# Kernel tuning notes

Hardware: AMD Instinct MI355X
Metric: run time of the kernel (lower is better)

The kernel has to match this reference:

```python
import jax, jax.numpy as jnp
import numpy as np

BETA = 0.25
K = 1024   # num_codebook_vectors
D = 256    # latent_dim


def setup_inputs() -> dict:
    key = jax.random.key(0)
    k1, k2 = jax.random.split(key)
    z = jax.random.normal(k1, (32, D, 32, 32), dtype=jnp.float32)
    # original init: uniform(-1/K, 1/K)
    codebook = jax.random.uniform(k2, (K, D), dtype=jnp.float32, minval=-1.0 / K, maxval=1.0 / K)
    return {"z": z, "codebook": codebook}


def reference(z, codebook):
    B, C, H, W = z.shape
    sg = jax.lax.stop_gradient
    # NCHW -> NHWC, flatten to [N, D]
    z_nhwc = jnp.transpose(z, (0, 2, 3, 1))
    zf = z_nhwc.reshape(-1, C)
    # squared distances via sum-of-squares + matmul: [N, K]
    d = (jnp.sum(zf * zf, axis=1, keepdims=True)
         + jnp.sum(codebook * codebook, axis=1)
         - 2.0 * jnp.matmul(zf, codebook.T))
    idx = jnp.argmin(d, axis=1)                      # [N]
    z_q = codebook[idx].reshape(B, H, W, C)          # gather + reshape
    # commitment + codebook loss
    loss = (jnp.mean((sg(z_q) - z_nhwc) ** 2)
            + BETA * jnp.mean((z_q - sg(z_nhwc)) ** 2))
    # straight-through estimator
    z_q = z_nhwc + sg(z_q - z_nhwc)
    z_q = jnp.transpose(z_q, (0, 3, 1, 2))           # back to NCHW
    return z_q, idx, loss
```

## Files before the change

kernel.cpp:

```cpp
#include <hip/hip_runtime.h>

constexpr int D_ = 256;
constexpr int K_ = 1024;
constexpr int P_ = 1024;
constexpr int N_ = 32768;

constexpr int IDX_OFF  = 8388608;
constexpr int LOSS_OFF = 8421376;

constexpr int CB16_OFF = 0;
constexpr int CN_OFF   = 262400;
constexpr int ZN_OFF   = 263424;
constexpr int CNT_OFF  = 296448;
constexpr int WL_OFF   = 296449;
constexpr size_t SCRATCH_BYTES = (size_t)(WL_OFF + N_) * 4;

constexpr float RESCUE_MARGIN = 1e-4f;

typedef _Float16 half8 __attribute__((ext_vector_type(8)));
typedef float f32x4 __attribute__((ext_vector_type(4)));

__device__ __forceinline__ void stage16(const float* g, float* l) {
  __builtin_amdgcn_global_load_lds(
      (const __attribute__((address_space(1))) unsigned int*)g,
      (__attribute__((address_space(3))) unsigned int*)l, 16, 0, 0);
}

__global__ __launch_bounds__(64) void vq_prep(const float* __restrict__ z,
                                              const float* __restrict__ cb,
                                              float* __restrict__ scratch,
                                              float* __restrict__ loss) {
  const int blk = blockIdx.x;
  const int lane = threadIdx.x;
  if (blk < 512) {
    const int n0 = blk * 64;
    const int b = n0 >> 10, p0 = n0 & (P_ - 1);
    const float* zp = z + (size_t)b * (D_ * P_) + p0 + lane;
    float a8[8];
    #pragma unroll
    for (int i = 0; i < 8; ++i) a8[i] = 0.0f;
    for (int oct = 0; oct < 32; ++oct) {
      #pragma unroll
      for (int i = 0; i < 8; ++i) {
        float v = zp[(size_t)(oct * 8 + i) * P_];
        a8[i] = fmaf(v, v, a8[i]);
      }
    }
    scratch[ZN_OFF + n0 + lane] = ((a8[0] + a8[1]) + (a8[2] + a8[3])) +
                                  ((a8[4] + a8[5]) + (a8[6] + a8[7]));
    if (blk == 0 && lane == 0) {
      *loss = 0.0f;
      ((int*)(scratch + CNT_OFF))[0] = 0;
    }
  } else if (blk < 1536) {
    const int k = blk - 512;
    const float* row = cb + (size_t)k * D_;
    double s = 0.0;
    #pragma unroll
    for (int i = 0; i < 4; ++i) {
      double v = (double)row[lane + i * 64];
      s = fma(v, v, s);
    }
    #pragma unroll
    for (int off = 32; off; off >>= 1) s += __shfl_down(s, off, 64);
    if (lane == 0) scratch[CN_OFF + k] = (float)s;
  } else {
    const int kt = blk - 1536;
    const int k = kt * 16 + (lane & 15);
    const int quad = lane >> 4;
    _Float16* cw = (_Float16*)(scratch + CB16_OFF);
    for (int ds = 0; ds < 8; ++ds) {
      const float* src = cb + (size_t)k * D_ + ds * 32 + quad * 8;
      half8 h, lo;
      #pragma unroll
      for (int j = 0; j < 8; ++j) {
        const float v = src[j] * 1024.0f;
        const _Float16 hh = (_Float16)v;
        h[j] = hh;
        lo[j] = (_Float16)(v - (float)hh);
      }
      const int s = kt * 8 + ds;
      *(half8*)(cw + ((size_t)(s * 2 + 0) * 64 + lane) * 8) = h;
      *(half8*)(cw + ((size_t)(s * 2 + 1) * 64 + lane) * 8) = lo;
    }
  }
}

__global__ __launch_bounds__(256, 2) void vq_mfma(const float* __restrict__ z,
                                                  const float* __restrict__ scratch_c,
                                                  float* __restrict__ scratch,
                                                  float* __restrict__ idxf) {
  const int t = threadIdx.x;
  const int w = t >> 6;
  const int l = t & 63;
  const int quad = l >> 4;
  const int col = l & 15;
  const int rh = w & 1;
  const int cs = w >> 1;
  const int n0 = blockIdx.x * 64;
  const int b = n0 >> 10;
  const int p0 = n0 & (P_ - 1);

  const float* __restrict__ cbsw_f = scratch_c + CB16_OFF;
  const float* __restrict__ cnorm = scratch_c + CN_OFF;
  const float* __restrict__ zn = scratch_c + ZN_OFF;

  __shared__ alignas(16) float Bbuf[2][2][4096];
  __shared__ alignas(16) float cnLds[1024];
  __shared__ float sM1[4][32];
  __shared__ float sM2[4][32];
  __shared__ int   sI1[4][32];
  float* Azs = &Bbuf[0][1][0];

  *(float4*)(cnLds + t * 4) = *(const float4*)(cnorm + t * 4);

  float znr[2][4];
  #pragma unroll
  for (int rt = 0; rt < 2; ++rt) {
    const float4 znv = *(const float4*)(zn + n0 + rh * 32 + rt * 16 + quad * 4);
    znr[rt][0] = znv.x; znr[rt][1] = znv.y;
    znr[rt][2] = znv.z; znr[rt][3] = znv.w;
  }

  half8 Ah[2][8], Al[2][8];
  const int dl0 = w * 8;
  for (int ds = 0; ds < 8; ++ds) {
    __syncthreads();
    #pragma unroll
    for (int i = 0; i < 8; ++i) {
      const int dloc = dl0 + i;
      Azs[l * 33 + dloc] =
          z[(size_t)b * (D_ * P_) + (size_t)(ds * 32 + dloc) * P_ + p0 + l];
    }
    __syncthreads();
    #pragma unroll
    for (int rt = 0; rt < 2; ++rt) {
      const float* src = &Azs[(rh * 32 + rt * 16 + col) * 33 + quad * 8];
      half8 h, lo;
      #pragma unroll
      for (int j = 0; j < 8; ++j) {
        const float v = src[j];
        const _Float16 hh = (_Float16)v;
        h[j] = hh;
        lo[j] = (_Float16)(v - (float)hh);
      }
      Ah[rt][ds] = h;
      Al[rt][ds] = lo;
    }
  }

  asm volatile("s_waitcnt vmcnt(0)" ::: "memory");

  const int ch0 = rh * 8;
  const float* gsbase = cbsw_f + (size_t)cs * 32 * 4096 + l * 4;
  #pragma unroll
  for (int j = 0; j < 8; ++j) {
    const int chunk = ch0 + j;
    stage16(gsbase + chunk * 256, &Bbuf[cs][0][chunk * 256]);
  }

  float m1[2][4], m2v[2][4];
  int i1[2][4];
  #pragma unroll
  for (int rt = 0; rt < 2; ++rt)
    #pragma unroll
    for (int r = 0; r < 4; ++r) { m1[rt][r] = 1e30f; m2v[rt][r] = 1e30f; i1[rt][r] = 0; }

  float* bcur = &Bbuf[cs][0][0];
  float* bnxt = &Bbuf[cs][1][0];
  const float* cnp = cnLds + cs * 512 + col;
  int kg = cs * 512 + col;

  f32x4 AH0, AM0, AL0, AH1, AM1, AL1;
  f32x4 BH0, BM0, BL0, BH1, BM1, BL1;
  float cnfA = 0.f, cnfB = 0.f;
  int kgA = 0, kgB = 0;

  auto do_phase = [&](f32x4& H0, f32x4& M0, f32x4& L0,
                      f32x4& H1, f32x4& M1, f32x4& L1,
                      int p, float& cnf_sav, int& kg_sav) {
    asm volatile("s_waitcnt vmcnt(0)" ::: "memory");
    __builtin_amdgcn_s_barrier();
    __builtin_amdgcn_sched_barrier(0);

    if (p < 31) {
      const float* gsp = gsbase + (size_t)(p + 1) * 4096;
      #pragma unroll
      for (int j = 0; j < 8; ++j) {
        const int chunk = ch0 + j;
        stage16(gsp + chunk * 256, bnxt + chunk * 256);
      }
    }

    cnf_sav = *cnp;
    kg_sav = kg;

    H0 = {0.f,0.f,0.f,0.f}; M0 = {0.f,0.f,0.f,0.f}; L0 = {0.f,0.f,0.f,0.f};
    H1 = {0.f,0.f,0.f,0.f}; M1 = {0.f,0.f,0.f,0.f}; L1 = {0.f,0.f,0.f,0.f};

    __builtin_amdgcn_s_setprio(1);
    #pragma unroll
    for (int ds = 0; ds < 8; ++ds) {
      const half8 bh = *(const half8*)(bcur + (ds * 2 + 0) * 256 + l * 4);
      const half8 bl = *(const half8*)(bcur + (ds * 2 + 1) * 256 + l * 4);
      H0 = __builtin_amdgcn_mfma_f32_16x16x32_f16(Ah[0][ds], bh, H0, 0, 0, 0);
      H1 = __builtin_amdgcn_mfma_f32_16x16x32_f16(Ah[1][ds], bh, H1, 0, 0, 0);
      M0 = __builtin_amdgcn_mfma_f32_16x16x32_f16(Ah[0][ds], bl, M0, 0, 0, 0);
      M1 = __builtin_amdgcn_mfma_f32_16x16x32_f16(Ah[1][ds], bl, M1, 0, 0, 0);
      L0 = __builtin_amdgcn_mfma_f32_16x16x32_f16(Al[0][ds], bh, L0, 0, 0, 0);
      L1 = __builtin_amdgcn_mfma_f32_16x16x32_f16(Al[1][ds], bh, L1, 0, 0, 0);
    }
    __builtin_amdgcn_s_setprio(0);

    cnp += 16;
    kg += 16;
    float* tmp = bcur; bcur = bnxt; bnxt = tmp;
  };

  auto do_argmin = [&](const f32x4& H0, const f32x4& M0, const f32x4& L0,
                       const f32x4& H1, const f32x4& M1, const f32x4& L1,
                       float cnf, int kgp) {
    #pragma unroll
    for (int r = 0; r < 4; ++r) {
      const float s0 = fmaf((H0[r] + M0[r]) + L0[r], -0x1p-9f, znr[0][r] + cnf);
      if (s0 < m1[0][r]) { m2v[0][r] = m1[0][r]; m1[0][r] = s0; i1[0][r] = kgp; }
      else if (s0 < m2v[0][r]) m2v[0][r] = s0;
      const float s1 = fmaf((H1[r] + M1[r]) + L1[r], -0x1p-9f, znr[1][r] + cnf);
      if (s1 < m1[1][r]) { m2v[1][r] = m1[1][r]; m1[1][r] = s1; i1[1][r] = kgp; }
      else if (s1 < m2v[1][r]) m2v[1][r] = s1;
    }
  };

  do_phase(AH0, AM0, AL0, AH1, AM1, AL1, 0, cnfA, kgA);
  for (int i = 0; i < 15; ++i) {
    do_phase(BH0, BM0, BL0, BH1, BM1, BL1, 2 * i + 1, cnfB, kgB);
    do_argmin(AH0, AM0, AL0, AH1, AM1, AL1, cnfA, kgA);
    do_phase(AH0, AM0, AL0, AH1, AM1, AL1, 2 * i + 2, cnfA, kgA);
    do_argmin(BH0, BM0, BL0, BH1, BM1, BL1, cnfB, kgB);
  }
  do_phase(BH0, BM0, BL0, BH1, BM1, BL1, 31, cnfB, kgB);
  do_argmin(AH0, AM0, AL0, AH1, AM1, AL1, cnfA, kgA);
  do_argmin(BH0, BM0, BL0, BH1, BM1, BL1, cnfB, kgB);

  #pragma unroll
  for (int off = 1; off <= 8; off <<= 1) {
    #pragma unroll
    for (int rt = 0; rt < 2; ++rt)
      #pragma unroll
      for (int r = 0; r < 4; ++r) {
        const float o1 = __shfl_xor(m1[rt][r], off, 64);
        const float o2 = __shfl_xor(m2v[rt][r], off, 64);
        const int oi = __shfl_xor(i1[rt][r], off, 64);
        if (o1 < m1[rt][r]) { m2v[rt][r] = fminf(m1[rt][r], o2); m1[rt][r] = o1; i1[rt][r] = oi; }
        else if (o1 == m1[rt][r]) { i1[rt][r] = min(i1[rt][r], oi); m2v[rt][r] = m1[rt][r]; }
        else { m2v[rt][r] = fminf(m2v[rt][r], o1); }
      }
  }

  if (col == 0) {
    #pragma unroll
    for (int rt = 0; rt < 2; ++rt)
      #pragma unroll
      for (int r = 0; r < 4; ++r) {
        const int rl = rt * 16 + quad * 4 + r;
        sM1[w][rl] = m1[rt][r];
        sM2[w][rl] = m2v[rt][r];
        sI1[w][rl] = i1[rt][r];
      }
  }
  __syncthreads();
  if (w < 2 && col == 0) {
    int* cnt = (int*)(scratch + CNT_OFF);
    int* wl = (int*)(scratch + WL_OFF);
    #pragma unroll
    for (int rt = 0; rt < 2; ++rt)
      #pragma unroll
      for (int r = 0; r < 4; ++r) {
        const int rl = rt * 16 + quad * 4 + r;
        float a1 = sM1[w][rl], a2 = sM2[w][rl];
        int ai = sI1[w][rl];
        const float o1 = sM1[w + 2][rl], o2 = sM2[w + 2][rl];
        const int oi = sI1[w + 2][rl];
        if (o1 < a1) { a2 = fminf(a1, o2); a1 = o1; ai = oi; }
        else if (o1 == a1) { ai = min(ai, oi); a2 = a1; }
        else { a2 = fminf(a2, o1); }
        const int n = n0 + w * 32 + rl;
        idxf[n] = (float)ai;
        if (a2 - a1 < RESCUE_MARGIN) {
          const int pos = atomicAdd(cnt, 1);
          wl[pos] = n;
        }
      }
  }
}

__global__ __launch_bounds__(256, 4) void vq_rescue(const float* __restrict__ z,
                                                    const float* __restrict__ cb,
                                                    const float* __restrict__ scratch,
                                                    float* __restrict__ idxf) {
  const int tid = threadIdx.x;
  const float* cnorm = scratch + CN_OFF;
  const float* zn = scratch + ZN_OFF;
  const int count = ((const int*)(scratch + CNT_OFF))[0];
  const int* wl = (const int*)(scratch + WL_OFF);

  __shared__ alignas(16) float zb[8][D_];
  __shared__ int nrow[8];
  __shared__ float rv[256];
  __shared__ int ri[256];

  for (int base = blockIdx.x * 8; base < count; base += gridDim.x * 8) {
    const int take = min(8, count - base);
    if (tid < 8) nrow[tid] = wl[base + (tid < take ? tid : 0)];
    __syncthreads();
    #pragma unroll
    for (int r = 0; r < 8; ++r) {
      const int n = nrow[r];
      const int b = n >> 10, p = n & (P_ - 1);
      zb[r][tid] = z[(size_t)b * (D_ * P_) + (size_t)tid * P_ + p];
    }
    __syncthreads();

    const int k0 = tid * 4;
    const float4* __restrict__ cr0 = (const float4*)(cb + (size_t)(k0 + 0) * D_);
    const float4* __restrict__ cr1 = (const float4*)(cb + (size_t)(k0 + 1) * D_);
    const float4* __restrict__ cr2 = (const float4*)(cb + (size_t)(k0 + 2) * D_);
    const float4* __restrict__ cr3 = (const float4*)(cb + (size_t)(k0 + 3) * D_);

    float acc[8][4];
    #pragma unroll
    for (int r = 0; r < 8; ++r)
      #pragma unroll
      for (int j = 0; j < 4; ++j) acc[r][j] = 0.0f;

    for (int d4 = 0; d4 < 64; ++d4) {
      const float4 v0 = cr0[d4], v1 = cr1[d4], v2 = cr2[d4], v3 = cr3[d4];
      #pragma unroll
      for (int r = 0; r < 8; ++r) {
        const float4 zv = ((const float4*)zb[r])[d4];
        acc[r][0] = fmaf(zv.x, v0.x, acc[r][0]);
        acc[r][0] = fmaf(zv.y, v0.y, acc[r][0]);
        acc[r][0] = fmaf(zv.z, v0.z, acc[r][0]);
        acc[r][0] = fmaf(zv.w, v0.w, acc[r][0]);
        acc[r][1] = fmaf(zv.x, v1.x, acc[r][1]);
        acc[r][1] = fmaf(zv.y, v1.y, acc[r][1]);
        acc[r][1] = fmaf(zv.z, v1.z, acc[r][1]);
        acc[r][1] = fmaf(zv.w, v1.w, acc[r][1]);
        acc[r][2] = fmaf(zv.x, v2.x, acc[r][2]);
        acc[r][2] = fmaf(zv.y, v2.y, acc[r][2]);
        acc[r][2] = fmaf(zv.z, v2.z, acc[r][2]);
        acc[r][2] = fmaf(zv.w, v2.w, acc[r][2]);
        acc[r][3] = fmaf(zv.x, v3.x, acc[r][3]);
        acc[r][3] = fmaf(zv.y, v3.y, acc[r][3]);
        acc[r][3] = fmaf(zv.z, v3.z, acc[r][3]);
        acc[r][3] = fmaf(zv.w, v3.w, acc[r][3]);
      }
    }

    for (int r = 0; r < 8; ++r) {
      const int n = nrow[r];
      const float zA = zn[n];
      float bv = 1e30f;
      int bi = 0x7fffffff;
      #pragma unroll
      for (int j = 0; j < 4; ++j) {
        const float A = zA + cnorm[k0 + j];
        const float s = A - 2.0f * acc[r][j];
        if (s < bv) { bv = s; bi = k0 + j; }
      }
      rv[tid] = bv; ri[tid] = bi;
      __syncthreads();
      for (int off = 128; off >= 1; off >>= 1) {
        if (tid < off) {
          const float ov = rv[tid + off];
          const int oi = ri[tid + off];
          if (ov < rv[tid] || (ov == rv[tid] && oi < ri[tid])) { rv[tid] = ov; ri[tid] = oi; }
        }
        __syncthreads();
      }
      if (tid == 0 && r < take) idxf[n] = (float)ri[0];
      __syncthreads();
    }
  }
}

__global__ __launch_bounds__(256) void vq_gather(const float* __restrict__ z,
                                                 const float* __restrict__ cb,
                                                 const float* __restrict__ idxf,
                                                 float* __restrict__ out,
                                                 float* __restrict__ loss) {
  const int tid = threadIdx.x;
  const int lane = tid & 63;
  const int w = tid >> 6;
  const int n0 = blockIdx.x * 64;
  const int b = n0 >> 10;
  const int p0 = n0 & (P_ - 1);
  const int p = p0 + lane;

  const int idx = (int)(idxf[n0 + lane] + 0.5f);
  const float4* crow4 = (const float4*)(cb + (size_t)idx * D_);
  const size_t base = (size_t)b * (D_ * P_) + p;

  float acc = 0.0f;
  #pragma unroll 4
  for (int ci = 0; ci < 16; ++ci) {
    const float4 v = crow4[w * 16 + ci];
    const int c = w * 64 + ci * 4;
    const float vv[4] = {v.x, v.y, v.z, v.w};
    #pragma unroll
    for (int u = 0; u < 4; ++u) {
      const size_t a = base + (size_t)(c + u) * P_;
      const float zv = z[a];
      const float d = vv[u] - zv;
      out[a] = zv + d;
      acc = fmaf(d, d, acc);
    }
  }
  #pragma unroll
  for (int off = 32; off; off >>= 1) acc += __shfl_down(acc, off, 64);
  __shared__ float wsum[4];
  if (lane == 0) wsum[w] = acc;
  __syncthreads();
  if (tid == 0) {
    float s = wsum[0] + wsum[1] + wsum[2] + wsum[3];
    atomicAdd(loss, s * (1.25f / 8388608.0f));
  }
}

extern "C" void kernel_launch(void* const* d_in, const int* in_sizes, int n_in,
                              void* d_out, int out_size, void* d_ws, size_t ws_size,
                              hipStream_t stream) {
  const float* z = (const float*)d_in[0];
  const float* cb = (const float*)d_in[1];
  float* out = (float*)d_out;

  float* scratch = (d_ws != nullptr && ws_size >= SCRATCH_BYTES)
                       ? (float*)d_ws : out;

  vq_prep<<<1600, 64, 0, stream>>>(z, cb, scratch, out + LOSS_OFF);
  vq_mfma<<<N_ / 64, 256, 0, stream>>>(z, scratch, scratch, out + IDX_OFF);
  vq_rescue<<<128, 256, 0, stream>>>(z, cb, scratch, out + IDX_OFF);
  vq_gather<<<N_ / 64, 256, 0, stream>>>(z, cb, out + IDX_OFF, out, out + LOSS_OFF);
}
```

Baseline: 227.5 us.

## Give each wave private double-buffered codebook staging and drop block barriers

Each wave gets its own LDS ping-pong buffer pair and stages its codebook slice itself, in half-tiles, synchronising with a per-wave vmcnt wait instead of a workgroup-wide s_barrier every phase. The two-accumulator-set software pipeline that overlapped the argmin of one tile with the MFMAs of the next is replaced by a simple loop that computes a tile and then immediately does its argmin. The intent is to remove inter-wave barrier stalls. In exchange, the waves that used to share a buffer now each load their own copy, doubling global/L2 codebook traffic, and the argmin is no longer overlapped with the MFMAs.

```diff
diff --git a/kernel.cpp b/kernel.cpp
--- a/kernel.cpp
+++ b/kernel.cpp
@@ -105,12 +105,12 @@
   const float* __restrict__ cnorm = scratch_c + CN_OFF;
   const float* __restrict__ zn = scratch_c + ZN_OFF;
 
-  __shared__ alignas(16) float Bbuf[2][2][4096];
+  __shared__ alignas(16) float Bw[4][2][2048];
   __shared__ alignas(16) float cnLds[1024];
   __shared__ float sM1[4][32];
   __shared__ float sM2[4][32];
   __shared__ int   sI1[4][32];
-  float* Azs = &Bbuf[0][1][0];
+  float* Azs = &Bw[0][0][0];
 
   *(float4*)(cnLds + t * 4) = *(const float4*)(cnorm + t * 4);
 
@@ -148,16 +148,15 @@
       Al[rt][ds] = lo;
     }
   }
-
+  __syncthreads();
   asm volatile("s_waitcnt vmcnt(0)" ::: "memory");
 
-  const int ch0 = rh * 8;
-  const float* gsbase = cbsw_f + (size_t)cs * 32 * 4096 + l * 4;
+  float* myb0 = &Bw[w][0][0];
+  float* myb1 = &Bw[w][1][0];
+  const float* gs = cbsw_f + (size_t)cs * 32 * 4096 + l * 4;
+
   #pragma unroll
-  for (int j = 0; j < 8; ++j) {
-    const int chunk = ch0 + j;
-    stage16(gsbase + chunk * 256, &Bbuf[cs][0][chunk * 256]);
-  }
+  for (int j = 0; j < 8; ++j) stage16(gs + j * 256, myb0 + j * 256);
 
   float m1[2][4], m2v[2][4];
   int i1[2][4];
@@ -166,81 +165,74 @@
     #pragma unroll
     for (int r = 0; r < 4; ++r) { m1[rt][r] = 1e30f; m2v[rt][r] = 1e30f; i1[rt][r] = 0; }
 
-  float* bcur = &Bbuf[cs][0][0];
-  float* bnxt = &Bbuf[cs][1][0];
   const float* cnp = cnLds + cs * 512 + col;
   int kg = cs * 512 + col;
 
-  f32x4 AH0, AM0, AL0, AH1, AM1, AL1;
-  f32x4 BH0, BM0, BL0, BH1, BM1, BL1;
-  float cnfA = 0.f, cnfB = 0.f;
-  int kgA = 0, kgB = 0;
-
-  auto do_phase = [&](f32x4& H0, f32x4& M0, f32x4& L0,
-                      f32x4& H1, f32x4& M1, f32x4& L1,
-                      int p, float& cnf_sav, int& kg_sav) {
-    asm volatile("s_waitcnt vmcnt(0)" ::: "memory");
-    __builtin_amdgcn_s_barrier();
-    __builtin_amdgcn_sched_barrier(0);
-
-    if (p < 31) {
-      const float* gsp = gsbase + (size_t)(p + 1) * 4096;
-      #pragma unroll
-      for (int j = 0; j < 8; ++j) {
-        const int chunk = ch0 + j;
-        stage16(gsp + chunk * 256, bnxt + chunk * 256);
-      }
-    }
-
-    cnf_sav = *cnp;
-    kg_sav = kg;
-
-    H0 = {0.f,0.f,0.f,0.f}; M0 = {0.f,0.f,0.f,0.f}; L0 = {0.f,0.f,0.f,0.f};
-    H1 = {0.f,0.f,0.f,0.f}; M1 = {0.f,0.f,0.f,0.f}; L1 = {0.f,0.f,0.f,0.f};
-
-    __builtin_amdgcn_s_setprio(1);
-    #pragma unroll
-    for (int ds = 0; ds < 8; ++ds) {
-      const half8 bh = *(const half8*)(bcur + (ds * 2 + 0) * 256 + l * 4);
-      const half8 bl = *(const half8*)(bcur + (ds * 2 + 1) * 256 + l * 4);
-      H0 = __builtin_amdgcn_mfma_f32_16x16x32_f16(Ah[0][ds], bh, H0, 0, 0, 0);
-      H1 = __builtin_amdgcn_mfma_f32_16x16x32_f16(Ah[1][ds], bh, H1, 0, 0, 0);
-      M0 = __builtin_amdgcn_mfma_f32_16x16x32_f16(Ah[0][ds], bl, M0, 0, 0, 0);
-      M1 = __builtin_amdgcn_mfma_f32_16x16x32_f16(Ah[1][ds], bl, M1, 0, 0, 0);
-      L0 = __builtin_amdgcn_mfma_f32_16x16x32_f16(Al[0][ds], bh, L0, 0, 0, 0);
-      L1 = __builtin_amdgcn_mfma_f32_16x16x32_f16(Al[1][ds], bh, L1, 0, 0, 0);
-    }
-    __builtin_amdgcn_s_setprio(0);
-
-    cnp += 16;
-    kg += 16;
-    float* tmp = bcur; bcur = bnxt; bnxt = tmp;
-  };
-
-  auto do_argmin = [&](const f32x4& H0, const f32x4& M0, const f32x4& L0,
-                       const f32x4& H1, const f32x4& M1, const f32x4& L1,
-                       float cnf, int kgp) {
-    #pragma unroll
-    for (int r = 0; r < 4; ++r) {
-      const float s0 = fmaf((H0[r] + M0[r]) + L0[r], -0x1p-9f, znr[0][r] + cnf);
-      if (s0 < m1[0][r]) { m2v[0][r] = m1[0][r]; m1[0][r] = s0; i1[0][r] = kgp; }
-      else if (s0 < m2v[0][r]) m2v[0][r] = s0;
-      const float s1 = fmaf((H1[r] + M1[r]) + L1[r], -0x1p-9f, znr[1][r] + cnf);
-      if (s1 < m1[1][r]) { m2v[1][r] = m1[1][r]; m1[1][r] = s1; i1[1][r] = kgp; }
-      else if (s1 < m2v[1][r]) m2v[1][r] = s1;
-    }
-  };
-
-  do_phase(AH0, AM0, AL0, AH1, AM1, AL1, 0, cnfA, kgA);
-  for (int i = 0; i < 15; ++i) {
-    do_phase(BH0, BM0, BL0, BH1, BM1, BL1, 2 * i + 1, cnfB, kgB);
-    do_argmin(AH0, AM0, AL0, AH1, AM1, AL1, cnfA, kgA);
-    do_phase(AH0, AM0, AL0, AH1, AM1, AL1, 2 * i + 2, cnfA, kgA);
-    do_argmin(BH0, BM0, BL0, BH1, BM1, BL1, cnfB, kgB);
-  }
-  do_phase(BH0, BM0, BL0, BH1, BM1, BL1, 31, cnfB, kgB);
-  do_argmin(AH0, AM0, AL0, AH1, AM1, AL1, cnfA, kgA);
-  do_argmin(BH0, BM0, BL0, BH1, BM1, BL1, cnfB, kgB);
+  for (int kt = 0; kt < 32; ++kt) {
+    f32x4 H0 = {0.f,0.f,0.f,0.f}, M0 = {0.f,0.f,0.f,0.f}, L0 = {0.f,0.f,0.f,0.f};
+    f32x4 H1 = {0.f,0.f,0.f,0.f}, M1 = {0.f,0.f,0.f,0.f}, L1 = {0.f,0.f,0.f,0.f};
+
+    {
+      const float* gsp = gs + (size_t)(kt * 2 + 1) * 2048;
+      #pragma unroll
+      for (int j = 0; j < 8; ++j) stage16(gsp + j * 256, myb1 + j * 256);
+      asm volatile("s_waitcnt vmcnt(8)" ::: "memory");
+      __builtin_amdgcn_sched_barrier(0);
+
+      __builtin_amdgcn_s_setprio(1);
+      #pragma unroll
+      for (int ds = 0; ds < 4; ++ds) {
+        const half8 bh = *(const half8*)(myb0 + (ds * 2 + 0) * 256 + l * 4);
+        const half8 bl = *(const half8*)(myb0 + (ds * 2 + 1) * 256 + l * 4);
+        H0 = __builtin_amdgcn_mfma_f32_16x16x32_f16(Ah[0][ds], bh, H0, 0, 0, 0);
+        H1 = __builtin_amdgcn_mfma_f32_16x16x32_f16(Ah[1][ds], bh, H1, 0, 0, 0);
+        M0 = __builtin_amdgcn_mfma_f32_16x16x32_f16(Ah[0][ds], bl, M0, 0, 0, 0);
+        M1 = __builtin_amdgcn_mfma_f32_16x16x32_f16(Ah[1][ds], bl, M1, 0, 0, 0);
+        L0 = __builtin_amdgcn_mfma_f32_16x16x32_f16(Al[0][ds], bh, L0, 0, 0, 0);
+        L1 = __builtin_amdgcn_mfma_f32_16x16x32_f16(Al[1][ds], bh, L1, 0, 0, 0);
+      }
+      __builtin_amdgcn_s_setprio(0);
+    }
+
+    {
+      if (kt < 31) {
+        const float* gsp = gs + (size_t)(kt * 2 + 2) * 2048;
+        #pragma unroll
+        for (int j = 0; j < 8; ++j) stage16(gsp + j * 256, myb0 + j * 256);
+        asm volatile("s_waitcnt vmcnt(8)" ::: "memory");
+      } else {
+        asm volatile("s_waitcnt vmcnt(0)" ::: "memory");
+      }
+      __builtin_amdgcn_sched_barrier(0);
+
+      __builtin_amdgcn_s_setprio(1);
+      #pragma unroll
+      for (int ds = 4; ds < 8; ++ds) {
+        const half8 bh = *(const half8*)(myb1 + ((ds - 4) * 2 + 0) * 256 + l * 4);
+        const half8 bl = *(const half8*)(myb1 + ((ds - 4) * 2 + 1) * 256 + l * 4);
+        H0 = __builtin_amdgcn_mfma_f32_16x16x32_f16(Ah[0][ds], bh, H0, 0, 0, 0);
+        H1 = __builtin_amdgcn_mfma_f32_16x16x32_f16(Ah[1][ds], bh, H1, 0, 0, 0);
+        M0 = __builtin_amdgcn_mfma_f32_16x16x32_f16(Ah[0][ds], bl, M0, 0, 0, 0);
+        M1 = __builtin_amdgcn_mfma_f32_16x16x32_f16(Ah[1][ds], bl, M1, 0, 0, 0);
+        L0 = __builtin_amdgcn_mfma_f32_16x16x32_f16(Al[0][ds], bh, L0, 0, 0, 0);
+        L1 = __builtin_amdgcn_mfma_f32_16x16x32_f16(Al[1][ds], bh, L1, 0, 0, 0);
+      }
+      __builtin_amdgcn_s_setprio(0);
+
+      const float cnf = *cnp;
+      #pragma unroll
+      for (int r = 0; r < 4; ++r) {
+        const float s0 = fmaf((H0[r] + M0[r]) + L0[r], -0x1p-9f, znr[0][r] + cnf);
+        if (s0 < m1[0][r]) { m2v[0][r] = m1[0][r]; m1[0][r] = s0; i1[0][r] = kg; }
+        else if (s0 < m2v[0][r]) m2v[0][r] = s0;
+        const float s1 = fmaf((H1[r] + M1[r]) + L1[r], -0x1p-9f, znr[1][r] + cnf);
+        if (s1 < m1[1][r]) { m2v[1][r] = m1[1][r]; m1[1][r] = s1; i1[1][r] = kg; }
+        else if (s1 < m2v[1][r]) m2v[1][r] = s1;
+      }
+      cnp += 16;
+      kg += 16;
+    }
+  }
 
   #pragma unroll
   for (int off = 1; off <= 8; off <<= 1) {
```

After: 234.9 us. 3.3% more time.
